# Performance work log

Measured on AMD Instinct MI355X. Metric: run time of the kernel, lower is better.

The kernel has to match this reference:

```python
import jax, jax.numpy as jnp
import numpy as np

B, T, DIM, FF, E, TOPK = 2, 2048, 1024, 4096, 8, 2


def setup_inputs() -> dict:
    key = jax.random.key(0)
    k0, k1, k2, k3 = jax.random.split(key, 4)
    x = jax.random.normal(k0, (B, T, DIM), jnp.float32)
    # router weight [E, D] (nn.Linear(dim, num_experts, bias=False))
    Wr = jax.random.normal(k1, (E, DIM), jnp.float32) * (DIM ** -0.5)
    # per-expert FFN weights, stacked: W1 [E, D, FF], W2 [E, FF, D]
    W1 = jax.random.normal(k2, (E, DIM, FF), jnp.float32) * (DIM ** -0.5)
    W2 = jax.random.normal(k3, (E, FF, DIM), jnp.float32) * (FF ** -0.5)
    return {"x": x, "Wr": Wr, "W1": W1, "W2": W2}


def reference(x, Wr, W1, W2):
    """MoEFeedForward.forward, world_size=1, STANDARD implementation.

    Math: per token, top_k experts by router logits, softmax over the top_k
    logits (fp32), y = sum_k w_k * FFN_{e_k}(x). The torch code realizes this
    via sort/permute + per-expert variable-size GEMM + weighted index_add;
    the scatter-add result is identical to the dense masked form below,
    which is the jit-friendly (static-shape) expression.
    """
    Bn, Tn, D = x.shape
    num_experts = Wr.shape[0]
    xf = x.reshape(-1, D)                      # [N, D], N = B*T
    N = xf.shape[0]

    logits = xf @ Wr.T                         # [N, E]
    topw, topi = jax.lax.top_k(logits, TOPK)   # [N, K]
    topw = jax.nn.softmax(topw.astype(jnp.float32), axis=-1).astype(x.dtype)

    # combine weight for each (token, expert): [N, E] (0 if not routed)
    combine = jnp.zeros((N, num_experts), x.dtype)
    combine = combine.at[jnp.arange(N)[:, None], topi].add(topw)

    out = jnp.zeros_like(xf)
    for e in range(num_experts):               # fixed small loop over experts
        h = jax.nn.gelu(xf @ W1[e], approximate=False)  # exact GELU (nn.GELU)
        out = out + combine[:, e:e + 1] * (h @ W2[e])
    return out.reshape(Bn, Tn, D)
```

## Files before the change

### kernel.cpp

```cpp
#include <hip/hip_runtime.h>
#include <hip/hip_bf16.h>
#include <hip/hip_fp16.h>

#define NTOK 4096
#define DIM 1024
#define FF 4096
#define NE 8
#define NSLOT 8192

typedef _Float16 half8 __attribute__((ext_vector_type(8)));
typedef _Float16 half4 __attribute__((ext_vector_type(4)));
typedef float floatx4 __attribute__((ext_vector_type(4)));

__device__ __forceinline__ float gelu_exact(float x) {
    return 0.5f * x * (1.0f + erff(x * 0.70710678118654752f));
}

__device__ __forceinline__ void gl_lds16(const void* g, void* l) {
    __builtin_amdgcn_global_load_lds(
        (const __attribute__((address_space(1))) void*)g,
        (__attribute__((address_space(3))) void*)l, 16, 0, 0);
}

__global__ __launch_bounds__(256) void k_convert_x(const float* __restrict__ x,
                                                   _Float16* __restrict__ xh) {
    int i = (blockIdx.x * 256 + threadIdx.x) * 8;
    float4 a = *(const float4*)(x + i);
    float4 b = *(const float4*)(x + i + 4);
    half8 h;
    h[0] = (_Float16)a.x; h[1] = (_Float16)a.y; h[2] = (_Float16)a.z; h[3] = (_Float16)a.w;
    h[4] = (_Float16)b.x; h[5] = (_Float16)b.y; h[6] = (_Float16)b.z; h[7] = (_Float16)b.w;
    *(half8*)(xh + i) = h;
}

__global__ __launch_bounds__(256) void k_transpose(const float* __restrict__ src,
                                                   _Float16* __restrict__ dst,
                                                   int R, int C) {
    __shared__ float t[64][65];
    int e = blockIdx.z;
    const float* s = src + (size_t)e * R * C;
    _Float16* d = dst + (size_t)e * C * R;
    int r0 = blockIdx.y * 64, c0 = blockIdx.x * 64;
    int tid = threadIdx.x;
    int rr = tid >> 4, cc = (tid & 15) * 4;
#pragma unroll
    for (int i = 0; i < 4; ++i) {
        float4 v = *(const float4*)(s + (size_t)(r0 + rr + i * 16) * C + c0 + cc);
        t[rr + i * 16][cc] = v.x; t[rr + i * 16][cc + 1] = v.y;
        t[rr + i * 16][cc + 2] = v.z; t[rr + i * 16][cc + 3] = v.w;
    }
    __syncthreads();
    int f = tid >> 3, ch = tid & 7;
#pragma unroll
    for (int j = 0; j < 2; ++j) {
        int fr = f + j * 32;
        half8 v;
#pragma unroll
        for (int u = 0; u < 8; ++u) v[u] = (_Float16)t[ch * 8 + u][fr];
        *(half8*)(d + (size_t)(c0 + fr) * R + r0 + ch * 8) = v;
    }
}

__global__ __launch_bounds__(256) void k_router(const float* __restrict__ x,
                                                const float* __restrict__ Wr,
                                                int* __restrict__ counts,
                                                int* __restrict__ tok_e,
                                                float* __restrict__ tok_w,
                                                int* __restrict__ tok_pos) {
    __shared__ float wr[NE * DIM];
    int tid = threadIdx.x;
    for (int i = tid; i < NE * DIM / 4; i += 256)
        ((float4*)wr)[i] = ((const float4*)Wr)[i];
    __syncthreads();

    int w = tid >> 6, lane = tid & 63;
    int t = blockIdx.x * 4 + w;

    float acc[NE] = {};
    for (int j = 0; j < DIM / 64; ++j) {
        float xv = x[t * DIM + j * 64 + lane];
#pragma unroll
        for (int e = 0; e < NE; ++e)
            acc[e] += xv * wr[e * DIM + j * 64 + lane];
    }
#pragma unroll
    for (int e = 0; e < NE; ++e) {
#pragma unroll
        for (int s = 32; s; s >>= 1) acc[e] += __shfl_xor(acc[e], s, 64);
    }
    if (lane == 0) {
        int b0 = 0; float m0 = acc[0];
#pragma unroll
        for (int e = 1; e < NE; ++e) { if (acc[e] > m0) { m0 = acc[e]; b0 = e; } }
        int b1 = -1; float m1 = -1e30f;
#pragma unroll
        for (int e = 0; e < NE; ++e) { if (e != b0 && acc[e] > m1) { m1 = acc[e]; b1 = e; } }
        float z = __expf(m1 - m0);
        float zz = 1.0f / (1.0f + z);
        int p0 = atomicAdd(&counts[b0], 1);
        int p1 = atomicAdd(&counts[b1], 1);
        tok_e[2 * t] = b0;  tok_e[2 * t + 1] = b1;
        tok_w[2 * t] = zz;  tok_w[2 * t + 1] = z * zz;
        tok_pos[2 * t] = p0; tok_pos[2 * t + 1] = p1;
    }
}

__global__ void k_prefix(const int* __restrict__ counts, int* __restrict__ offs,
                         int* __restrict__ tmap) {
    if (threadIdx.x == 0 && blockIdx.x == 0) {
        int s = 0, n = 0;
        for (int e = 0; e < NE; ++e) {
            offs[e] = s;
            int c = counts[e];
            for (int mt = 0; mt * 128 < c; ++mt) tmap[1 + n++] = (e << 16) | mt;
            s += c;
        }
        offs[NE] = s;
        tmap[0] = n;
    }
}

__global__ __launch_bounds__(256) void k_slots(const int* __restrict__ offs,
                                               const int* __restrict__ tok_e,
                                               const int* __restrict__ tok_pos,
                                               int* __restrict__ tok_slot,
                                               int* __restrict__ list_tok) {
    int idx = blockIdx.x * 256 + threadIdx.x;
    if (idx < NSLOT) {
        int e = tok_e[idx];
        int slot = offs[e] + tok_pos[idx];
        tok_slot[idx] = slot;
        list_tok[slot] = idx >> 1;
    }
}

template<int K, int NOUT, bool GATHER, bool GELU>
__global__ __launch_bounds__(256) void k_ffn(
    const _Float16* __restrict__ Abase,
    const _Float16* __restrict__ Wbase,
    const int* __restrict__ tmap,
    const int* __restrict__ counts,
    const int* __restrict__ offs,
    const int* __restrict__ list_tok,
    _Float16* __restrict__ Out) {

    int nt_m = tmap[0];
    if ((int)blockIdx.x >= nt_m) return;
    int ent = tmap[1 + blockIdx.x];
    int e = ent >> 16, mt = ent & 0xffff;
    int base = offs[e] + mt * 128;
    int valid = counts[e] - mt * 128;
    int f0 = blockIdx.y * 128;

    __shared__ _Float16 lds[32768];

    int tid = threadIdx.x;
    int wid = tid >> 6, lane = tid & 63;

    const char* AB = (const char*)Abase;
    const char* WB = (const char*)(Wbase + (size_t)e * NOUT * K);

    size_t aoff[4]; unsigned boff[4];
#pragma unroll
    for (int i = 0; i < 4; ++i) {
        int g = wid * 256 + i * 64 + lane;
        int r = g >> 3;
        int c = (g & 7) ^ (r & 7);
        int rr = (r < valid) ? r : (valid - 1);
        unsigned arow = GATHER ? (unsigned)list_tok[base + rr] : (unsigned)(base + rr);
        aoff[i] = (size_t)arow * (K * 2) + c * 16;
        boff[i] = (unsigned)(f0 + r) * (unsigned)(K * 2) + c * 16;
    }

    floatx4 acc[4][4];
#pragma unroll
    for (int m = 0; m < 4; ++m)
#pragma unroll
        for (int n = 0; n < 4; ++n) acc[m][n] = (floatx4){0.f, 0.f, 0.f, 0.f};

    int la = lane & 15, lb = lane >> 4;
    int wm = (wid >> 1) * 64, wn = (wid & 1) * 64;

#pragma unroll
    for (int i = 0; i < 4; ++i)
        gl_lds16(AB + aoff[i], lds + wid * 2048 + i * 512);
#pragma unroll
    for (int i = 0; i < 4; ++i)
        gl_lds16(WB + boff[i], lds + 16384 + wid * 2048 + i * 512);
    asm volatile("s_waitcnt vmcnt(0)" ::: "memory");
    __builtin_amdgcn_s_barrier();
    __builtin_amdgcn_sched_barrier(0);

    constexpr int NT = K / 64;
#pragma unroll 2
    for (int t = 0; t < NT; ++t) {
        int cur = t & 1;
        if (t + 1 < NT) {
            size_t kadv = (size_t)(t + 1) * 128;
            _Float16* Ad = lds + (cur ^ 1) * 8192;
            _Float16* Bd = lds + 16384 + (cur ^ 1) * 8192;
#pragma unroll
            for (int i = 0; i < 4; ++i)
                gl_lds16(AB + aoff[i] + kadv, Ad + wid * 2048 + i * 512);
#pragma unroll
            for (int i = 0; i < 4; ++i)
                gl_lds16(WB + boff[i] + kadv, Bd + wid * 2048 + i * 512);
        }
        const _Float16* Ac = lds + cur * 8192;
        const _Float16* Bc = lds + 16384 + cur * 8192;
#pragma unroll
        for (int kk = 0; kk < 2; ++kk) {
            half8 af[4], bf[4];
#pragma unroll
            for (int m = 0; m < 4; ++m) {
                int row = wm + m * 16 + la;
                int c = kk * 4 + lb;
                af[m] = *(const half8*)(Ac + row * 64 + ((c ^ (row & 7)) * 8));
            }
#pragma unroll
            for (int n = 0; n < 4; ++n) {
                int row = wn + n * 16 + la;
                int c = kk * 4 + lb;
                bf[n] = *(const half8*)(Bc + row * 64 + ((c ^ (row & 7)) * 8));
            }
#pragma unroll
            for (int m = 0; m < 4; ++m)
#pragma unroll
                for (int n = 0; n < 4; ++n)
                    acc[m][n] = __builtin_amdgcn_mfma_f32_16x16x32_f16(af[m], bf[n], acc[m][n], 0, 0, 0);
        }
        __builtin_amdgcn_sched_barrier(0);
        asm volatile("s_waitcnt vmcnt(0)" ::: "memory");
        __builtin_amdgcn_s_barrier();
        __builtin_amdgcn_sched_barrier(0);
    }

    _Float16* tw = lds + wid * 4096;
#pragma unroll
    for (int m = 0; m < 4; ++m)
#pragma unroll
        for (int n = 0; n < 4; ++n) {
            floatx4 v = acc[m][n];
#pragma unroll
            for (int i = 0; i < 4; ++i) {
                float fv = v[i];
                if (GELU) fv = gelu_exact(fv);
                tw[(m * 16 + lb * 4 + i) * 64 + n * 16 + la] = (_Float16)fv;
            }
        }
#pragma unroll
    for (int i = 0; i < 8; ++i) {
        int gi = i * 64 + lane;
        int row = gi >> 3, c8 = gi & 7;
        half8 v = *(const half8*)(tw + gi * 8);
        int trow = wm + row;
        if (trow < valid)
            *(half8*)(Out + (size_t)(base + trow) * NOUT + f0 + wn + c8 * 8) = v;
    }
}

__global__ __launch_bounds__(256) void k_combine(const _Float16* __restrict__ yh,
                                                 const int* __restrict__ tok_slot,
                                                 const float* __restrict__ tok_w,
                                                 float* __restrict__ out) {
    int t = blockIdx.x;
    int d = threadIdx.x * 4;
    int s0 = tok_slot[2 * t], s1 = tok_slot[2 * t + 1];
    float w0 = tok_w[2 * t], w1 = tok_w[2 * t + 1];
    half4 y0 = *(const half4*)(yh + (size_t)s0 * DIM + d);
    half4 y1 = *(const half4*)(yh + (size_t)s1 * DIM + d);
    float4 o;
    o.x = w0 * (float)y0[0] + w1 * (float)y1[0];
    o.y = w0 * (float)y0[1] + w1 * (float)y1[1];
    o.z = w0 * (float)y0[2] + w1 * (float)y1[2];
    o.w = w0 * (float)y0[3] + w1 * (float)y1[3];
    *(float4*)(out + (size_t)t * DIM + d) = o;
}

extern "C" void kernel_launch(void* const* d_in, const int* in_sizes, int n_in,
                              void* d_out, int out_size, void* d_ws, size_t ws_size,
                              hipStream_t stream) {
    const float* x  = (const float*)d_in[0];
    const float* Wr = (const float*)d_in[1];
    const float* W1 = (const float*)d_in[2];
    const float* W2 = (const float*)d_in[3];
    float* out = (float*)d_out;

    char* ws = (char*)d_ws;
    _Float16* w1t  = (_Float16*)ws;
    _Float16* w2t  = (_Float16*)ws;
    _Float16* xh   = (_Float16*)(ws + 67108864);
    _Float16* hbuf = (_Float16*)(ws + 75497472);
    _Float16* yh   = (_Float16*)(ws + 142606336);
    char* p = ws + 159383552;
    int*   counts   = (int*)p;        p += 256;
    int*   offs     = (int*)p;        p += 256;
    int*   tmap     = (int*)p;        p += 512;
    int*   tok_e    = (int*)p;        p += NSLOT * 4;
    float* tok_w    = (float*)p;      p += NSLOT * 4;
    int*   tok_pos  = (int*)p;        p += NSLOT * 4;
    int*   tok_slot = (int*)p;        p += NSLOT * 4;
    int*   list_tok = (int*)p;        p += NSLOT * 4;

    hipMemsetAsync(counts, 0, NE * sizeof(int), stream);
    k_convert_x<<<NTOK * DIM / (256 * 8), 256, 0, stream>>>(x, xh);
    k_router<<<NTOK / 4, 256, 0, stream>>>(x, Wr, counts, tok_e, tok_w, tok_pos);
    k_prefix<<<1, 64, 0, stream>>>(counts, offs, tmap);
    k_slots<<<NSLOT / 256, 256, 0, stream>>>(offs, tok_e, tok_pos, tok_slot, list_tok);
    k_transpose<<<dim3(FF / 64, DIM / 64, NE), 256, 0, stream>>>(W1, w1t, DIM, FF);
    k_ffn<DIM, FF, true, true>
        <<<dim3(NSLOT / 128 + NE, FF / 128), 256, 0, stream>>>(
            xh, w1t, tmap, counts, offs, list_tok, hbuf);
    k_transpose<<<dim3(DIM / 64, FF / 64, NE), 256, 0, stream>>>(W2, w2t, FF, DIM);
    k_ffn<FF, DIM, false, false>
        <<<dim3(NSLOT / 128 + NE, DIM / 128), 256, 0, stream>>>(
            hbuf, w2t, tmap, counts, offs, list_tok, yh);
    k_combine<<<NTOK, 256, 0, stream>>>(yh, tok_slot, tok_w, out);
}
```

Measured before the change: 460.6 us.

## Use 256x256 tile FFN GEMM kernel with split-K for second GEMM

Adds a 512-thread kernel that computes 256x256 output tiles with 8x4 MFMA fragments per wave, so each A and B tile loaded into LDS is reused across more math. The first GEMM switches to this kernel. The second GEMM (K=4096, only 1024 outputs) is split along K into up to 4 partial fp16 buffers, chosen by available workspace, to raise the number of blocks, and the combine kernel sums the partials. The cost is more register pressure, extra partial-buffer traffic, fp16 rounding of the partial sums, and fewer M-tiles per expert with more padding waste.

```diff
diff --git a/kernel.cpp b/kernel.cpp
--- a/kernel.cpp
+++ b/kernel.cpp
@@ -106,17 +106,19 @@
 }
 
 __global__ void k_prefix(const int* __restrict__ counts, int* __restrict__ offs,
-                         int* __restrict__ tmap) {
+                         int* __restrict__ tmap256, int* __restrict__ tmap128) {
     if (threadIdx.x == 0 && blockIdx.x == 0) {
-        int s = 0, n = 0;
+        int s = 0, n2 = 0, n1 = 0;
         for (int e = 0; e < NE; ++e) {
             offs[e] = s;
             int c = counts[e];
-            for (int mt = 0; mt * 128 < c; ++mt) tmap[1 + n++] = (e << 16) | mt;
+            for (int mt = 0; mt * 256 < c; ++mt) tmap256[1 + n2++] = (e << 16) | mt;
+            for (int mt = 0; mt * 128 < c; ++mt) tmap128[1 + n1++] = (e << 16) | mt;
             s += c;
         }
         offs[NE] = s;
-        tmap[0] = n;
+        tmap256[0] = n2;
+        tmap128[0] = n1;
     }
 }
 
@@ -134,6 +136,138 @@
     }
 }
 
+template<int K, int NOUT, int KSPAN, bool GATHER, bool GELU>
+__global__ __launch_bounds__(512, 2) void k_ffn256(
+    const _Float16* __restrict__ Abase,
+    const _Float16* __restrict__ Wbase,
+    const int* __restrict__ tmap,
+    const int* __restrict__ counts,
+    const int* __restrict__ offs,
+    const int* __restrict__ list_tok,
+    _Float16* __restrict__ Out) {
+
+    int nt_m = tmap[0];
+    if ((int)blockIdx.x >= nt_m) return;
+    int ent = tmap[1 + blockIdx.x];
+    int e = ent >> 16, mt = ent & 0xffff;
+    int base = offs[e] + mt * 256;
+    int valid = counts[e] - mt * 256;
+    int f0 = blockIdx.y * 256;
+    int kbase = blockIdx.z * KSPAN;
+    Out += (size_t)blockIdx.z * ((size_t)NSLOT * NOUT);
+
+    __shared__ _Float16 lds[65536];
+
+    int tid = threadIdx.x;
+    int wid = tid >> 6, lane = tid & 63;
+
+    const char* AB = (const char*)Abase;
+    const char* WB = (const char*)(Wbase + (size_t)e * NOUT * K);
+
+    size_t aoff[4]; unsigned boff[4];
+#pragma unroll
+    for (int i = 0; i < 4; ++i) {
+        int g = i * 512 + tid;
+        int r = g >> 3;
+        int c = (g & 7) ^ (r & 7);
+        int rr = (r < valid) ? r : (valid - 1);
+        unsigned arow = GATHER ? (unsigned)list_tok[base + rr] : (unsigned)(base + rr);
+        aoff[i] = (size_t)arow * (K * 2) + c * 16 + (size_t)kbase * 2;
+        boff[i] = (unsigned)(f0 + r) * (unsigned)(K * 2) + c * 16 + (unsigned)kbase * 2;
+    }
+
+    floatx4 acc[8][4];
+#pragma unroll
+    for (int m = 0; m < 8; ++m)
+#pragma unroll
+        for (int n = 0; n < 4; ++n) acc[m][n] = (floatx4){0.f, 0.f, 0.f, 0.f};
+
+    int la = lane & 15, lb = lane >> 4;
+    int wmb = (wid >> 2) * 128, wnb = (wid & 3) * 64;
+
+#pragma unroll
+    for (int i = 0; i < 4; ++i)
+        gl_lds16(AB + aoff[i], lds + i * 4096 + wid * 512);
+#pragma unroll
+    for (int i = 0; i < 4; ++i)
+        gl_lds16(WB + boff[i], lds + 32768 + i * 4096 + wid * 512);
+    asm volatile("s_waitcnt vmcnt(0)" ::: "memory");
+    __builtin_amdgcn_s_barrier();
+    __builtin_amdgcn_sched_barrier(0);
+
+    constexpr int NT = KSPAN / 64;
+#pragma unroll 2
+    for (int t = 0; t < NT; ++t) {
+        int cur = t & 1;
+        if (t + 1 < NT) {
+            size_t adv = (size_t)(t + 1) * 128;
+            _Float16* Ad = lds + (cur ^ 1) * 16384;
+            _Float16* Bd = lds + 32768 + (cur ^ 1) * 16384;
+#pragma unroll
+            for (int i = 0; i < 4; ++i)
+                gl_lds16(AB + aoff[i] + adv, Ad + i * 4096 + wid * 512);
+#pragma unroll
+            for (int i = 0; i < 4; ++i)
+                gl_lds16(WB + boff[i] + adv, Bd + i * 4096 + wid * 512);
+        }
+        const _Float16* Ac = lds + cur * 16384;
+        const _Float16* Bc = lds + 32768 + cur * 16384;
+#pragma unroll
+        for (int kk = 0; kk < 2; ++kk) {
+            half8 af[8], bf[4];
+#pragma unroll
+            for (int n = 0; n < 4; ++n) {
+                int row = wnb + n * 16 + la;
+                int c = kk * 4 + lb;
+                bf[n] = *(const half8*)(Bc + row * 64 + ((c ^ (row & 7)) * 8));
+            }
+#pragma unroll
+            for (int m = 0; m < 8; ++m) {
+                int row = wmb + m * 16 + la;
+                int c = kk * 4 + lb;
+                af[m] = *(const half8*)(Ac + row * 64 + ((c ^ (row & 7)) * 8));
+            }
+#pragma unroll
+            for (int m = 0; m < 8; ++m)
+#pragma unroll
+                for (int n = 0; n < 4; ++n)
+                    acc[m][n] = __builtin_amdgcn_mfma_f32_16x16x32_f16(af[m], bf[n], acc[m][n], 0, 0, 0);
+        }
+        __builtin_amdgcn_sched_barrier(0);
+        asm volatile("s_waitcnt vmcnt(0)" ::: "memory");
+        __builtin_amdgcn_s_barrier();
+        __builtin_amdgcn_sched_barrier(0);
+    }
+
+    _Float16* tw = lds + wid * 4096;
+#pragma unroll
+    for (int ps = 0; ps < 2; ++ps) {
+#pragma unroll
+        for (int fi = 0; fi < 4; ++fi)
+#pragma unroll
+            for (int nf = 0; nf < 4; ++nf) {
+                floatx4 v = acc[ps * 4 + fi][nf];
+#pragma unroll
+                for (int i2 = 0; i2 < 4; ++i2) {
+                    float fv = v[i2];
+                    if (GELU) fv = gelu_exact(fv);
+                    tw[(fi * 16 + lb * 4 + i2) * 64 + nf * 16 + la] = (_Float16)fv;
+                }
+            }
+        asm volatile("s_waitcnt lgkmcnt(0)" ::: "memory");
+        __builtin_amdgcn_sched_barrier(0);
+#pragma unroll
+        for (int i2 = 0; i2 < 8; ++i2) {
+            int gi = i2 * 64 + lane;
+            int row = gi >> 3, c8 = gi & 7;
+            half8 v = *(const half8*)(tw + gi * 8);
+            int trow = wmb + ps * 64 + row;
+            if (trow < valid)
+                *(half8*)(Out + (size_t)(base + trow) * NOUT + f0 + wnb + c8 * 8) = v;
+        }
+    }
+}
+
 template<int K, int NOUT, bool GATHER, bool GELU>
 __global__ __launch_bounds__(256) void k_ffn(
     const _Float16* __restrict__ Abase,
@@ -248,6 +382,8 @@
                 tw[(m * 16 + lb * 4 + i) * 64 + n * 16 + la] = (_Float16)fv;
             }
         }
+    asm volatile("s_waitcnt lgkmcnt(0)" ::: "memory");
+    __builtin_amdgcn_sched_barrier(0);
 #pragma unroll
     for (int i = 0; i < 8; ++i) {
         int gi = i * 64 + lane;
@@ -259,21 +395,30 @@
     }
 }
 
-__global__ __launch_bounds__(256) void k_combine(const _Float16* __restrict__ yh,
+__global__ __launch_bounds__(256) void k_combine(const _Float16* __restrict__ yp,
                                                  const int* __restrict__ tok_slot,
                                                  const float* __restrict__ tok_w,
-                                                 float* __restrict__ out) {
+                                                 float* __restrict__ out,
+                                                 int nsplit) {
     int t = blockIdx.x;
     int d = threadIdx.x * 4;
     int s0 = tok_slot[2 * t], s1 = tok_slot[2 * t + 1];
     float w0 = tok_w[2 * t], w1 = tok_w[2 * t + 1];
-    half4 y0 = *(const half4*)(yh + (size_t)s0 * DIM + d);
-    half4 y1 = *(const half4*)(yh + (size_t)s1 * DIM + d);
+    float4 sum0 = {0.f, 0.f, 0.f, 0.f}, sum1 = {0.f, 0.f, 0.f, 0.f};
+    for (int z = 0; z < nsplit; ++z) {
+        const _Float16* p = yp + (size_t)z * NSLOT * DIM;
+        half4 y0 = *(const half4*)(p + (size_t)s0 * DIM + d);
+        half4 y1 = *(const half4*)(p + (size_t)s1 * DIM + d);
+        sum0.x += (float)y0[0]; sum0.y += (float)y0[1];
+        sum0.z += (float)y0[2]; sum0.w += (float)y0[3];
+        sum1.x += (float)y1[0]; sum1.y += (float)y1[1];
+        sum1.z += (float)y1[2]; sum1.w += (float)y1[3];
+    }
     float4 o;
-    o.x = w0 * (float)y0[0] + w1 * (float)y1[0];
-    o.y = w0 * (float)y0[1] + w1 * (float)y1[1];
-    o.z = w0 * (float)y0[2] + w1 * (float)y1[2];
-    o.w = w0 * (float)y0[3] + w1 * (float)y1[3];
+    o.x = w0 * sum0.x + w1 * sum1.x;
+    o.y = w0 * sum0.y + w1 * sum1.y;
+    o.z = w0 * sum0.z + w1 * sum1.z;
+    o.w = w0 * sum0.w + w1 * sum1.w;
     *(float4*)(out + (size_t)t * DIM + d) = o;
 }
 
@@ -291,29 +436,46 @@
     _Float16* w2t  = (_Float16*)ws;
     _Float16* xh   = (_Float16*)(ws + 67108864);
     _Float16* hbuf = (_Float16*)(ws + 75497472);
-    _Float16* yh   = (_Float16*)(ws + 142606336);
-    char* p = ws + 159383552;
-    int*   counts   = (int*)p;        p += 256;
-    int*   offs     = (int*)p;        p += 256;
-    int*   tmap     = (int*)p;        p += 512;
+    char* p = ws + 142606336;
+    int*   counts   = (int*)p;        p += 1024;
+    int*   offs     = (int*)p;        p += 1024;
+    int*   tmap256  = (int*)p;        p += 1024;
+    int*   tmap128  = (int*)p;        p += 1024;
     int*   tok_e    = (int*)p;        p += NSLOT * 4;
     float* tok_w    = (float*)p;      p += NSLOT * 4;
     int*   tok_pos  = (int*)p;        p += NSLOT * 4;
     int*   tok_slot = (int*)p;        p += NSLOT * 4;
     int*   list_tok = (int*)p;        p += NSLOT * 4;
+    const size_t OFF_Y = 142606336 + 196608;
+    const size_t SZ_Y  = (size_t)NSLOT * DIM * 2;
+    _Float16* yp = (_Float16*)(ws + OFF_Y);
+
+    int nsplit = (ws_size >= OFF_Y + 4 * SZ_Y) ? 4
+               : (ws_size >= OFF_Y + 2 * SZ_Y) ? 2 : 1;
 
     hipMemsetAsync(counts, 0, NE * sizeof(int), stream);
     k_convert_x<<<NTOK * DIM / (256 * 8), 256, 0, stream>>>(x, xh);
     k_router<<<NTOK / 4, 256, 0, stream>>>(x, Wr, counts, tok_e, tok_w, tok_pos);
-    k_prefix<<<1, 64, 0, stream>>>(counts, offs, tmap);
+    k_prefix<<<1, 64, 0, stream>>>(counts, offs, tmap256, tmap128);
     k_slots<<<NSLOT / 256, 256, 0, stream>>>(offs, tok_e, tok_pos, tok_slot, list_tok);
+
     k_transpose<<<dim3(FF / 64, DIM / 64, NE), 256, 0, stream>>>(W1, w1t, DIM, FF);
-    k_ffn<DIM, FF, true, true>
-        <<<dim3(NSLOT / 128 + NE, FF / 128), 256, 0, stream>>>(
-            xh, w1t, tmap, counts, offs, list_tok, hbuf);
+    k_ffn256<DIM, FF, DIM, true, true>
+        <<<dim3(NSLOT / 256 + NE, FF / 256), 512, 0, stream>>>(
+            xh, w1t, tmap256, counts, offs, list_tok, hbuf);
     k_transpose<<<dim3(DIM / 64, FF / 64, NE), 256, 0, stream>>>(W2, w2t, FF, DIM);
-    k_ffn<FF, DIM, false, false>
-        <<<dim3(NSLOT / 128 + NE, DIM / 128), 256, 0, stream>>>(
-            hbuf, w2t, tmap, counts, offs, list_tok, yh);
-    k_combine<<<NTOK, 256, 0, stream>>>(yh, tok_slot, tok_w, out);
-}
+    if (nsplit == 4) {
+        k_ffn256<FF, DIM, 1024, false, false>
+            <<<dim3(NSLOT / 256 + NE, DIM / 256, 4), 512, 0, stream>>>(
+                hbuf, w2t, tmap256, counts, offs, list_tok, yp);
+    } else if (nsplit == 2) {
+        k_ffn256<FF, DIM, 2048, false, false>
+            <<<dim3(NSLOT / 256 + NE, DIM / 256, 2), 512, 0, stream>>>(
+                hbuf, w2t, tmap256, counts, offs, list_tok, yp);
+    } else {
+        k_ffn<FF, DIM, false, false>
+            <<<dim3(NSLOT / 128 + NE, DIM / 128), 256, 0, stream>>>(
+                hbuf, w2t, tmap128, counts, offs, list_tok, yp);
+    }
+    k_combine<<<NTOK, 256, 0, stream>>>(yp, tok_slot, tok_w, out, nsplit);
+}
```

Result: faster. 433.7 us (-5.8%).
